# Performance work log

Hardware: AMD Instinct MI355X
Metric: run time of the kernel (lower is better)

Reference implementation:

```python
import jax, jax.numpy as jnp
import numpy as np

EPS = 1e-6
N_HEADS = 16

def setup_inputs() -> dict:
    key = jax.random.key(0)
    ks = jax.random.split(key, 5)
    B, N, D = 64, 512, 1024
    x = jax.random.normal(ks[0], (B, N, D), dtype=jnp.float32)
    s = 0.02
    W_q = jax.random.normal(ks[1], (D, D), dtype=jnp.float32) * s
    W_k = jax.random.normal(ks[2], (D, D), dtype=jnp.float32) * s
    W_v = jax.random.normal(ks[3], (D, D), dtype=jnp.float32) * s
    W_o = jax.random.normal(ks[4], (D, D), dtype=jnp.float32) * s
    z = jnp.zeros((D,), dtype=jnp.float32)
    return {"x": x, "W_q": W_q, "b_q": z, "W_k": W_k, "b_k": z,
            "W_v": W_v, "b_v": z, "W_o": W_o, "b_o": z}

def _heads(t, B, N, H, Dk):
    # [B,N,H*Dk] -> [B,H,N,Dk]
    return t.reshape(B, N, H, Dk).transpose(0, 2, 1, 3)

def reference(x, W_q, b_q, W_k, b_k, W_v, b_v, W_o, b_o):
    B, N, Dm = x.shape
    H = N_HEADS
    Dk = Dm // H
    q = _heads(x @ W_q.T + b_q, B, N, H, Dk)
    k = _heads(x @ W_k.T + b_k, B, N, H, Dk)
    v = _heads(x @ W_v.T + b_v, B, N, H, Dk)
    # position decay LUT: exp(-n/N), applied to ReLU feature maps of q and k
    dec = jnp.exp(-jnp.arange(N, dtype=jnp.float32) / N)[None, None, :, None]
    qf = jax.nn.relu(q) * dec  # [B,H,N,Dk]
    kf = jax.nn.relu(k) * dec
    # global (non-causal) summaries: KV = sum_n k_n v_n^T, Ksum = sum_n k_n
    KV = jnp.einsum('bhnd,bhne->bhde', kf, v)      # [B,H,Dk,Dk]
    Ksum = kf.sum(axis=2)                           # [B,H,Dk]
    denom = jnp.einsum('bhnd,bhd->bhn', qf, Ksum) + EPS
    out = jnp.einsum('bhnd,bhde->bhne', qf, KV) / denom[..., None]
    out = out.transpose(0, 2, 1, 3).reshape(B, N, Dm)
    return out @ W_o.T + b_o
```

## Files before the change

kernel.cpp:

```cpp
#include <hip/hip_runtime.h>
#include <hip/hip_bf16.h>

typedef __attribute__((ext_vector_type(8))) __bf16 bf16x8;
typedef __attribute__((ext_vector_type(4))) __bf16 bf16x4;
typedef __attribute__((ext_vector_type(4))) float f32x4;

#define NBATCH 64
#define NSEQ   512
#define DMODEL 1024
#define NHEAD  16
#define DHEAD  64
#define MROWS  (NBATCH * NSEQ)

static __device__ __forceinline__ void gload_lds16(const void* gp, void* lp) {
  __builtin_amdgcn_global_load_lds(
      (__attribute__((address_space(1))) const void*)gp,
      (__attribute__((address_space(3))) void*)lp,
      16, 0, 0);
}

__global__ void cvt_kernel(const float* __restrict__ in, __bf16* __restrict__ out, int n4) {
  int i = blockIdx.x * blockDim.x + threadIdx.x;
  int stride = gridDim.x * blockDim.x;
  for (; i < n4; i += stride) {
    const float4 v = reinterpret_cast<const float4*>(in)[i];
    bf16x4 o;
    o.x = (__bf16)v.x; o.y = (__bf16)v.y; o.z = (__bf16)v.z; o.w = (__bf16)v.w;
    reinterpret_cast<bf16x4*>(out)[i] = o;
  }
}

template <int MODE>
__global__ __launch_bounds__(512, 1)
void gemm256_kernel(const __bf16* __restrict__ A, const __bf16* __restrict__ Bw,
                    const float* __restrict__ bias0, const float* __restrict__ bias1,
                    const float* __restrict__ bias2,
                    __bf16* __restrict__ outq, __bf16* __restrict__ outkT,
                    __bf16* __restrict__ outvT, float* __restrict__ outf) {
  extern __shared__ char smem[];
  constexpr int K = 1024;
  constexpr int NT = K / 64;
  constexpr int NBN = (MODE == 0) ? 12 : 4;
  constexpr int NWG = 128 * NBN;
  constexpr int CPX = NWG / 8;

  const int raw = blockIdx.x;
  const int wgid = (raw & 7) * CPX + (raw >> 3);
  const int bm = wgid / NBN;
  const int bn = wgid - bm * NBN;
  const int m0 = bm * 256, j0 = bn * 256;

  const int tid = threadIdx.x;
  const int l = tid & 63;
  const int w = tid >> 6;
  const int wm = w >> 2, wn = w & 3;
  const int lrow = l & 15, g16 = l >> 4;

  f32x4 acc[8][4] = {};

  auto stage = [&](int part, int tileIdx) {
    const int mat = part >> 1, kh = part & 1;
    const int buf = tileIdx & 1;
    char* region = smem + (((buf << 2) | (mat << 1) | kh) << 14);
    const __bf16* src = mat ? Bw : A;
    const int rowbase = mat ? j0 : m0;
    const int kk = tileIdx * 64 + kh * 32;
#pragma unroll
    for (int i = 0; i < 2; i++) {
      const int Q = i * 8192 + tid * 16;
      const int Ls = Q ^ (((Q >> 7) & 3) << 4);
      gload_lds16(src + (size_t)(rowbase + (Ls >> 6)) * K + kk + ((Ls & 63) >> 1),
                  region + Q);
    }
  };

  auto ldfrag = [&](int mat, int kh, int buf, int row) -> bf16x8 {
    const int L = row * 64 + g16 * 16;
    const int phys = L ^ (((row >> 1) & 3) << 4);
    return *reinterpret_cast<const bf16x8*>(
        smem + (((buf << 2) | (mat << 1) | kh) << 14) + phys);
  };

  stage(0, 0); stage(2, 0); stage(3, 0); stage(1, 0);
  stage(0, 1); stage(2, 1);
  asm volatile("s_waitcnt vmcnt(4)" ::: "memory");
  __builtin_amdgcn_s_barrier();

  const int arow = wm * 128 + lrow;
  const int brow = wn * 64 + lrow;

  for (int T = 0; T < NT; T++) {
    const int buf = T & 1;
    bf16x8 a00[4], bk0[4], a10[4];
#pragma unroll
    for (int mi = 0; mi < 4; mi++) a00[mi] = ldfrag(0, 0, buf, arow + mi * 16);
#pragma unroll
    for (int ni = 0; ni < 4; ni++) bk0[ni] = ldfrag(1, 0, buf, brow + ni * 16);
#pragma unroll
    for (int mi = 0; mi < 4; mi++) a10[mi] = ldfrag(0, 0, buf, arow + 64 + mi * 16);
    if (T + 1 < NT) stage(3, T + 1);
    __builtin_amdgcn_s_barrier();
    __builtin_amdgcn_s_setprio(1);
#pragma unroll
    for (int mi = 0; mi < 4; mi++)
#pragma unroll
      for (int ni = 0; ni < 4; ni++)
        acc[mi][ni] = __builtin_amdgcn_mfma_f32_16x16x32_bf16(a00[mi], bk0[ni], acc[mi][ni], 0, 0, 0);
    __builtin_amdgcn_s_setprio(0);
    __builtin_amdgcn_s_barrier();
    bf16x8 a01[4], bk1[4], a11[4];
#pragma unroll
    for (int mi = 0; mi < 4; mi++) a01[mi] = ldfrag(0, 1, buf, arow + mi * 16);
#pragma unroll
    for (int ni = 0; ni < 4; ni++) bk1[ni] = ldfrag(1, 1, buf, brow + ni * 16);
#pragma unroll
    for (int mi = 0; mi < 4; mi++) a11[mi] = ldfrag(0, 1, buf, arow + 64 + mi * 16);
    if (T + 1 < NT) stage(1, T + 1);
    __builtin_amdgcn_s_barrier();
    __builtin_amdgcn_s_setprio(1);
#pragma unroll
    for (int mi = 0; mi < 4; mi++)
#pragma unroll
      for (int ni = 0; ni < 4; ni++)
        acc[4 + mi][ni] = __builtin_amdgcn_mfma_f32_16x16x32_bf16(a10[mi], bk0[ni], acc[4 + mi][ni], 0, 0, 0);
    __builtin_amdgcn_s_setprio(0);
    __builtin_amdgcn_s_barrier();
    if (T + 2 < NT) stage(0, T + 2);
    __builtin_amdgcn_s_barrier();
    __builtin_amdgcn_s_setprio(1);
#pragma unroll
    for (int mi = 0; mi < 4; mi++)
#pragma unroll
      for (int ni = 0; ni < 4; ni++)
        acc[mi][ni] = __builtin_amdgcn_mfma_f32_16x16x32_bf16(a01[mi], bk1[ni], acc[mi][ni], 0, 0, 0);
    __builtin_amdgcn_s_setprio(0);
    __builtin_amdgcn_s_barrier();
    if (T + 2 < NT) stage(2, T + 2);
    __builtin_amdgcn_s_barrier();
    __builtin_amdgcn_s_setprio(1);
#pragma unroll
    for (int mi = 0; mi < 4; mi++)
#pragma unroll
      for (int ni = 0; ni < 4; ni++)
        acc[4 + mi][ni] = __builtin_amdgcn_mfma_f32_16x16x32_bf16(a11[mi], bk1[ni], acc[4 + mi][ni], 0, 0, 0);
    __builtin_amdgcn_s_setprio(0);
    if (T < NT - 2)       asm volatile("s_waitcnt vmcnt(4)" ::: "memory");
    else if (T == NT - 2) asm volatile("s_waitcnt vmcnt(0)" ::: "memory");
    __builtin_amdgcn_s_barrier();
  }

  if constexpr (MODE == 0) {
    const int sel = j0 >> 10;
    const int jb = j0 & 1023;
    const float* bias = (sel == 0) ? bias0 : ((sel == 1) ? bias1 : bias2);
#pragma unroll
    for (int mi = 0; mi < 8; mi++) {
      const int mbase = m0 + wm * 128 + mi * 16 + g16 * 4;
#pragma unroll
      for (int ni = 0; ni < 4; ni++) {
        const int j = jb + wn * 64 + ni * 16 + lrow;
        const float bv_ = bias[j];
        if (sel == 0) {
#pragma unroll
          for (int r = 0; r < 4; r++) {
            const int m = mbase + r;
            float val = acc[mi][ni][r] + bv_;
            val = fmaxf(val, 0.f) * __expf(-(float)(m & (NSEQ - 1)) * (1.0f / NSEQ));
            outq[(size_t)m * DMODEL + j] = (__bf16)val;
          }
        } else {
          const int bidx = mbase >> 9;
          const int n0 = mbase & (NSEQ - 1);
          __bf16* dst = (sel == 1) ? outkT : outvT;
          bf16x4 pk;
#pragma unroll
          for (int r = 0; r < 4; r++) {
            float val = acc[mi][ni][r] + bv_;
            if (sel == 1)
              val = fmaxf(val, 0.f) * __expf(-(float)(n0 + r) * (1.0f / NSEQ));
            pk[r] = (__bf16)val;
          }
          *reinterpret_cast<bf16x4*>(
              &dst[((size_t)((bidx * NHEAD + (j >> 6)) * DHEAD + (j & 63))) * NSEQ + n0]) = pk;
        }
      }
    }
  } else {
#pragma unroll
    for (int mi = 0; mi < 8; mi++) {
      const int mbase = m0 + wm * 128 + mi * 16 + g16 * 4;
#pragma unroll
      for (int ni = 0; ni < 4; ni++) {
        const int j = j0 + wn * 64 + ni * 16 + lrow;
        const float bo = bias0[j];
#pragma unroll
        for (int r = 0; r < 4; r++)
          outf[(size_t)(mbase + r) * DMODEL + j] = acc[mi][ni][r] + bo;
      }
    }
  }
}

__global__ void attn_kernel(const __bf16* __restrict__ qf, const __bf16* __restrict__ kfT,
                            const __bf16* __restrict__ vT, __bf16* __restrict__ attn) {
  const int bh = blockIdx.x;
  const int b = bh >> 4, h = bh & 15;
  const __bf16* kT = kfT + (size_t)bh * DHEAD * NSEQ;
  const __bf16* vTp = vT + (size_t)bh * DHEAD * NSEQ;
  const __bf16* qp = qf + (size_t)b * NSEQ * DMODEL + h * DHEAD;
  __bf16* op = attn + (size_t)b * NSEQ * DMODEL + h * DHEAD;

  const int tid = threadIdx.x;
  const int l = tid & 63;
  const int w = tid >> 6;
  const int lrow = l & 15, lk = (l >> 4) * 8;

  __shared__ __bf16 KVT[64][88];
  __shared__ float Ksum[64];
  __shared__ float ksum_part[4][64];
  __shared__ float denom[512];

  {
    f32x4 kv[4] = {};
    const int arow = w * 16 + lrow;
    for (int kk = 0; kk < NSEQ; kk += 32) {
      bf16x8 a = *reinterpret_cast<const bf16x8*>(&kT[(size_t)arow * NSEQ + kk + lk]);
#pragma unroll
      for (int ni = 0; ni < 4; ni++) {
        bf16x8 bv = *reinterpret_cast<const bf16x8*>(&vTp[(size_t)(ni * 16 + lrow) * NSEQ + kk + lk]);
        kv[ni] = __builtin_amdgcn_mfma_f32_16x16x32_bf16(a, bv, kv[ni], 0, 0, 0);
      }
    }
    const int d0 = w * 16 + ((l >> 4) << 2);
#pragma unroll
    for (int ni = 0; ni < 4; ni++) {
      const int e = ni * 16 + lrow;
      bf16x4 pk;
#pragma unroll
      for (int r = 0; r < 4; r++) pk[r] = (__bf16)kv[ni][r];
      *reinterpret_cast<bf16x4*>(&KVT[e][d0]) = pk;
    }
  }

  {
    const int d = tid & 63, part = tid >> 6;
    float s = 0.f;
    for (int n = part * 128; n < part * 128 + 128; n += 8) {
      bf16x8 kv8 = *reinterpret_cast<const bf16x8*>(&kT[(size_t)d * NSEQ + n]);
#pragma unroll
      for (int j = 0; j < 8; j++) s += (float)kv8[j];
    }
    ksum_part[part][d] = s;
  }
  __syncthreads();
  if (tid < 64)
    Ksum[tid] = ksum_part[0][tid] + ksum_part[1][tid] + ksum_part[2][tid] + ksum_part[3][tid];
  __syncthreads();

  for (int n = tid; n < NSEQ; n += 256) {
    float s = 0.f;
#pragma unroll
    for (int d = 0; d < DHEAD; d += 8) {
      bf16x8 q8 = *reinterpret_cast<const bf16x8*>(&qp[(size_t)n * DMODEL + d]);
#pragma unroll
      for (int j = 0; j < 8; j++) s += (float)q8[j] * Ksum[d + j];
    }
    denom[n] = s + 1e-6f;
  }
  __syncthreads();

  for (int t = 0; t < 8; t++) {
    const int nrow = t * 64 + w * 16 + lrow;
    bf16x8 a0 = *reinterpret_cast<const bf16x8*>(&qp[(size_t)nrow * DMODEL + lk]);
    bf16x8 a1 = *reinterpret_cast<const bf16x8*>(&qp[(size_t)nrow * DMODEL + 32 + lk]);
    f32x4 o[4] = {};
#pragma unroll
    for (int ni = 0; ni < 4; ni++) {
      bf16x8 b0 = *reinterpret_cast<const bf16x8*>(&KVT[ni * 16 + lrow][lk]);
      bf16x8 b1 = *reinterpret_cast<const bf16x8*>(&KVT[ni * 16 + lrow][32 + lk]);
      o[ni] = __builtin_amdgcn_mfma_f32_16x16x32_bf16(a0, b0, o[ni], 0, 0, 0);
      o[ni] = __builtin_amdgcn_mfma_f32_16x16x32_bf16(a1, b1, o[ni], 0, 0, 0);
    }
    const int n0 = t * 64 + w * 16 + ((l >> 4) << 2);
#pragma unroll
    for (int ni = 0; ni < 4; ni++) {
      const int e = ni * 16 + lrow;
#pragma unroll
      for (int r = 0; r < 4; r++)
        op[(size_t)(n0 + r) * DMODEL + e] = (__bf16)(o[ni][r] / denom[n0 + r]);
    }
  }
}

extern "C" void kernel_launch(void* const* d_in, const int* in_sizes, int n_in,
                              void* d_out, int out_size, void* d_ws, size_t ws_size,
                              hipStream_t stream) {
  (void)in_sizes; (void)n_in; (void)out_size; (void)ws_size;
  const float* x  = (const float*)d_in[0];
  const float* Wq = (const float*)d_in[1];
  const float* bq = (const float*)d_in[2];
  const float* Wk = (const float*)d_in[3];
  const float* bk = (const float*)d_in[4];
  const float* Wv = (const float*)d_in[5];
  const float* bv = (const float*)d_in[6];
  const float* Wo = (const float*)d_in[7];
  const float* bo = (const float*)d_in[8];
  float* out = (float*)d_out;

  char* ws = (char*)d_ws;
  __bf16* xb    = (__bf16*)(ws);
  __bf16* qf    = (__bf16*)(ws + 67108864);
  __bf16* kfT   = (__bf16*)(ws + 134217728);
  __bf16* vT    = (__bf16*)(ws + 201326592);
  __bf16* Wqkvb = (__bf16*)(ws + 268435456);
  __bf16* Wob   = (__bf16*)(ws + 274726912);
  __bf16* attnb = xb;

  cvt_kernel<<<4096, 256, 0, stream>>>(x, xb, (MROWS * DMODEL) / 4);
  cvt_kernel<<<1024, 256, 0, stream>>>(Wq, Wqkvb,                 (DMODEL * DMODEL) / 4);
  cvt_kernel<<<1024, 256, 0, stream>>>(Wk, Wqkvb + DMODEL * DMODEL,     (DMODEL * DMODEL) / 4);
  cvt_kernel<<<1024, 256, 0, stream>>>(Wv, Wqkvb + 2 * DMODEL * DMODEL, (DMODEL * DMODEL) / 4);
  cvt_kernel<<<1024, 256, 0, stream>>>(Wo, Wob, (DMODEL * DMODEL) / 4);

  gemm256_kernel<0><<<1536, 512, 131072, stream>>>(xb, Wqkvb, bq, bk, bv,
                                                   qf, kfT, vT, nullptr);
  attn_kernel<<<NBATCH * NHEAD, 256, 0, stream>>>(qf, kfT, vT, attnb);
  gemm256_kernel<1><<<512, 512, 131072, stream>>>(attnb, Wob, bo, nullptr, nullptr,
                                                  nullptr, nullptr, nullptr, out);
}
```

Measured before the change: 451.0 us.

## Simplify GEMM pipeline to one-ahead prefetch, fuse conversion kernels, hoist epilogue math

Replaces the two-tile-ahead staggered prefetch schedule, with many barriers, by a one-tile-ahead prefetch per iteration and a single wait and barrier at the end of each iteration. Merges the five fp32->bf16 conversion launches into one kernel. Hoists the bias loads and decay exponentials out of the inner epilogue loops. Fewer barriers reduce synchronisation overhead. The shorter prefetch distance and the full vmcnt(0) wait may expose global load latency.

```diff
diff --git a/kernel.cpp b/kernel.cpp
--- a/kernel.cpp
+++ b/kernel.cpp
@@ -19,14 +19,26 @@
       16, 0, 0);
 }
 
-__global__ void cvt_kernel(const float* __restrict__ in, __bf16* __restrict__ out, int n4) {
+__global__ void cvt_all_kernel(const float* __restrict__ x, const float* __restrict__ Wq,
+                               const float* __restrict__ Wk, const float* __restrict__ Wv,
+                               const float* __restrict__ Wo,
+                               __bf16* __restrict__ xb, __bf16* __restrict__ Wqkvb,
+                               __bf16* __restrict__ Wob) {
+  constexpr int NX = (MROWS * DMODEL) / 4;
+  constexpr int NW = (DMODEL * DMODEL) / 4;
   int i = blockIdx.x * blockDim.x + threadIdx.x;
-  int stride = gridDim.x * blockDim.x;
-  for (; i < n4; i += stride) {
-    const float4 v = reinterpret_cast<const float4*>(in)[i];
+  const int stride = gridDim.x * blockDim.x;
+  for (; i < NX + 4 * NW; i += stride) {
+    const float* src; __bf16* dst; int idx;
+    if (i < NX)            { src = x;  dst = xb;             idx = i; }
+    else if (i < NX + NW)  { src = Wq; dst = Wqkvb;          idx = i - NX; }
+    else if (i < NX + 2*NW){ src = Wk; dst = Wqkvb + 4*NW;   idx = i - NX - NW; }
+    else if (i < NX + 3*NW){ src = Wv; dst = Wqkvb + 8*NW;   idx = i - NX - 2*NW; }
+    else                   { src = Wo; dst = Wob;            idx = i - NX - 3*NW; }
+    const float4 v = reinterpret_cast<const float4*>(src)[idx];
     bf16x4 o;
     o.x = (__bf16)v.x; o.y = (__bf16)v.y; o.z = (__bf16)v.z; o.w = (__bf16)v.w;
-    reinterpret_cast<bf16x4*>(out)[i] = o;
+    reinterpret_cast<bf16x4*>(dst)[idx] = o;
   }
 }
 
@@ -82,8 +94,7 @@
   };
 
   stage(0, 0); stage(2, 0); stage(3, 0); stage(1, 0);
-  stage(0, 1); stage(2, 1);
-  asm volatile("s_waitcnt vmcnt(4)" ::: "memory");
+  asm volatile("s_waitcnt vmcnt(0)" ::: "memory");
   __builtin_amdgcn_s_barrier();
 
   const int arow = wm * 128 + lrow;
@@ -91,93 +102,100 @@
 
   for (int T = 0; T < NT; T++) {
     const int buf = T & 1;
-    bf16x8 a00[4], bk0[4], a10[4];
-#pragma unroll
-    for (int mi = 0; mi < 4; mi++) a00[mi] = ldfrag(0, 0, buf, arow + mi * 16);
-#pragma unroll
-    for (int ni = 0; ni < 4; ni++) bk0[ni] = ldfrag(1, 0, buf, brow + ni * 16);
-#pragma unroll
-    for (int mi = 0; mi < 4; mi++) a10[mi] = ldfrag(0, 0, buf, arow + 64 + mi * 16);
-    if (T + 1 < NT) stage(3, T + 1);
-    __builtin_amdgcn_s_barrier();
+    const bool pre = (T + 1 < NT);
+    if (pre) { stage(0, T + 1); stage(2, T + 1); }
+    bf16x8 a0[4], b0[4], a1[4];
+#pragma unroll
+    for (int mi = 0; mi < 4; mi++) a0[mi] = ldfrag(0, 0, buf, arow + mi * 16);
+#pragma unroll
+    for (int ni = 0; ni < 4; ni++) b0[ni] = ldfrag(1, 0, buf, brow + ni * 16);
+#pragma unroll
+    for (int mi = 0; mi < 4; mi++) a1[mi] = ldfrag(0, 0, buf, arow + 64 + mi * 16);
+    if (pre) { stage(3, T + 1); stage(1, T + 1); }
     __builtin_amdgcn_s_setprio(1);
 #pragma unroll
     for (int mi = 0; mi < 4; mi++)
 #pragma unroll
       for (int ni = 0; ni < 4; ni++)
-        acc[mi][ni] = __builtin_amdgcn_mfma_f32_16x16x32_bf16(a00[mi], bk0[ni], acc[mi][ni], 0, 0, 0);
+        acc[mi][ni] = __builtin_amdgcn_mfma_f32_16x16x32_bf16(a0[mi], b0[ni], acc[mi][ni], 0, 0, 0);
     __builtin_amdgcn_s_setprio(0);
-    __builtin_amdgcn_s_barrier();
-    bf16x8 a01[4], bk1[4], a11[4];
-#pragma unroll
-    for (int mi = 0; mi < 4; mi++) a01[mi] = ldfrag(0, 1, buf, arow + mi * 16);
-#pragma unroll
-    for (int ni = 0; ni < 4; ni++) bk1[ni] = ldfrag(1, 1, buf, brow + ni * 16);
-#pragma unroll
-    for (int mi = 0; mi < 4; mi++) a11[mi] = ldfrag(0, 1, buf, arow + 64 + mi * 16);
-    if (T + 1 < NT) stage(1, T + 1);
-    __builtin_amdgcn_s_barrier();
+    bf16x8 a0n[4];
+#pragma unroll
+    for (int mi = 0; mi < 4; mi++) a0n[mi] = ldfrag(0, 1, buf, arow + mi * 16);
     __builtin_amdgcn_s_setprio(1);
 #pragma unroll
     for (int mi = 0; mi < 4; mi++)
 #pragma unroll
       for (int ni = 0; ni < 4; ni++)
-        acc[4 + mi][ni] = __builtin_amdgcn_mfma_f32_16x16x32_bf16(a10[mi], bk0[ni], acc[4 + mi][ni], 0, 0, 0);
+        acc[4 + mi][ni] = __builtin_amdgcn_mfma_f32_16x16x32_bf16(a1[mi], b0[ni], acc[4 + mi][ni], 0, 0, 0);
     __builtin_amdgcn_s_setprio(0);
-    __builtin_amdgcn_s_barrier();
-    if (T + 2 < NT) stage(0, T + 2);
-    __builtin_amdgcn_s_barrier();
+    bf16x8 b1[4], a1n[4];
+#pragma unroll
+    for (int ni = 0; ni < 4; ni++) b1[ni] = ldfrag(1, 1, buf, brow + ni * 16);
+#pragma unroll
+    for (int mi = 0; mi < 4; mi++) a1n[mi] = ldfrag(0, 1, buf, arow + 64 + mi * 16);
     __builtin_amdgcn_s_setprio(1);
 #pragma unroll
     for (int mi = 0; mi < 4; mi++)
 #pragma unroll
       for (int ni = 0; ni < 4; ni++)
-        acc[mi][ni] = __builtin_amdgcn_mfma_f32_16x16x32_bf16(a01[mi], bk1[ni], acc[mi][ni], 0, 0, 0);
+        acc[mi][ni] = __builtin_amdgcn_mfma_f32_16x16x32_bf16(a0n[mi], b1[ni], acc[mi][ni], 0, 0, 0);
+#pragma unroll
+    for (int mi = 0; mi < 4; mi++)
+#pragma unroll
+      for (int ni = 0; ni < 4; ni++)
+        acc[4 + mi][ni] = __builtin_amdgcn_mfma_f32_16x16x32_bf16(a1n[mi], b1[ni], acc[4 + mi][ni], 0, 0, 0);
     __builtin_amdgcn_s_setprio(0);
-    __builtin_amdgcn_s_barrier();
-    if (T + 2 < NT) stage(2, T + 2);
-    __builtin_amdgcn_s_barrier();
-    __builtin_amdgcn_s_setprio(1);
-#pragma unroll
-    for (int mi = 0; mi < 4; mi++)
-#pragma unroll
-      for (int ni = 0; ni < 4; ni++)
-        acc[4 + mi][ni] = __builtin_amdgcn_mfma_f32_16x16x32_bf16(a11[mi], bk1[ni], acc[4 + mi][ni], 0, 0, 0);
-    __builtin_amdgcn_s_setprio(0);
-    if (T < NT - 2)       asm volatile("s_waitcnt vmcnt(4)" ::: "memory");
-    else if (T == NT - 2) asm volatile("s_waitcnt vmcnt(0)" ::: "memory");
-    __builtin_amdgcn_s_barrier();
+    if (pre) {
+      asm volatile("s_waitcnt vmcnt(0)" ::: "memory");
+      __builtin_amdgcn_s_barrier();
+    }
   }
 
   if constexpr (MODE == 0) {
     const int sel = j0 >> 10;
     const int jb = j0 & 1023;
     const float* bias = (sel == 0) ? bias0 : ((sel == 1) ? bias1 : bias2);
-#pragma unroll
-    for (int mi = 0; mi < 8; mi++) {
-      const int mbase = m0 + wm * 128 + mi * 16 + g16 * 4;
-#pragma unroll
-      for (int ni = 0; ni < 4; ni++) {
-        const int j = jb + wn * 64 + ni * 16 + lrow;
-        const float bv_ = bias[j];
-        if (sel == 0) {
-#pragma unroll
-          for (int r = 0; r < 4; r++) {
-            const int m = mbase + r;
-            float val = acc[mi][ni][r] + bv_;
-            val = fmaxf(val, 0.f) * __expf(-(float)(m & (NSEQ - 1)) * (1.0f / NSEQ));
+    float bj[4];
+#pragma unroll
+    for (int ni = 0; ni < 4; ni++) bj[ni] = bias[jb + wn * 64 + ni * 16 + lrow];
+    if (sel == 0) {
+#pragma unroll
+      for (int mi = 0; mi < 8; mi++) {
+        const int mbase = m0 + wm * 128 + mi * 16 + g16 * 4;
+#pragma unroll
+        for (int r = 0; r < 4; r++) {
+          const int m = mbase + r;
+          const float dec = __expf(-(float)(m & (NSEQ - 1)) * (1.0f / NSEQ));
+#pragma unroll
+          for (int ni = 0; ni < 4; ni++) {
+            const int j = jb + wn * 64 + ni * 16 + lrow;
+            const float val = fmaxf(acc[mi][ni][r] + bj[ni], 0.f) * dec;
             outq[(size_t)m * DMODEL + j] = (__bf16)val;
           }
-        } else {
-          const int bidx = mbase >> 9;
-          const int n0 = mbase & (NSEQ - 1);
-          __bf16* dst = (sel == 1) ? outkT : outvT;
+        }
+      }
+    } else {
+#pragma unroll
+      for (int mi = 0; mi < 8; mi++) {
+        const int mbase = m0 + wm * 128 + mi * 16 + g16 * 4;
+        const int bidx = mbase >> 9;
+        const int n0 = mbase & (NSEQ - 1);
+        float dec4[4];
+        if (sel == 1) {
+#pragma unroll
+          for (int r = 0; r < 4; r++)
+            dec4[r] = __expf(-(float)(n0 + r) * (1.0f / NSEQ));
+        }
+        __bf16* dst = (sel == 1) ? outkT : outvT;
+#pragma unroll
+        for (int ni = 0; ni < 4; ni++) {
+          const int j = jb + wn * 64 + ni * 16 + lrow;
           bf16x4 pk;
 #pragma unroll
           for (int r = 0; r < 4; r++) {
-            float val = acc[mi][ni][r] + bv_;
-            if (sel == 1)
-              val = fmaxf(val, 0.f) * __expf(-(float)(n0 + r) * (1.0f / NSEQ));
+            float val = acc[mi][ni][r] + bj[ni];
+            if (sel == 1) val = fmaxf(val, 0.f) * dec4[r];
             pk[r] = (__bf16)val;
           }
           *reinterpret_cast<bf16x4*>(
@@ -316,11 +334,7 @@
   __bf16* Wob   = (__bf16*)(ws + 274726912);
   __bf16* attnb = xb;
 
-  cvt_kernel<<<4096, 256, 0, stream>>>(x, xb, (MROWS * DMODEL) / 4);
-  cvt_kernel<<<1024, 256, 0, stream>>>(Wq, Wqkvb,                 (DMODEL * DMODEL) / 4);
-  cvt_kernel<<<1024, 256, 0, stream>>>(Wk, Wqkvb + DMODEL * DMODEL,     (DMODEL * DMODEL) / 4);
-  cvt_kernel<<<1024, 256, 0, stream>>>(Wv, Wqkvb + 2 * DMODEL * DMODEL, (DMODEL * DMODEL) / 4);
-  cvt_kernel<<<1024, 256, 0, stream>>>(Wo, Wob, (DMODEL * DMODEL) / 4);
+  cvt_all_kernel<<<4096, 256, 0, stream>>>(x, Wq, Wk, Wv, Wo, xb, Wqkvb, Wob);
 
   gemm256_kernel<0><<<1536, 512, 131072, stream>>>(xb, Wqkvb, bq, bk, bv,
                                                    qf, kfT, vT, nullptr);
```

New measurement: 437.7 us. 2.9% less time.
